# Performance work log

Measured on AMD Instinct MI355X. Metric: run time of the kernel, lower is better.

## Reference

```python
import jax, jax.numpy as jnp
import numpy as np


def _sobel_filters():
    # 3D Sobel kernels for x, y, z directions, shape (3, 1, 3, 3, 3) in OIDHW.
    x = np.array([[[-1, 0, 1], [-2, 0, 2], [-1, 0, 1]],
                  [[-2, 0, 2], [-4, 0, 4], [-2, 0, 2]],
                  [[-1, 0, 1], [-2, 0, 2], [-1, 0, 1]]], dtype=np.float32)
    y = np.array([[[1, 2, 1], [0, 0, 0], [-1, -2, -1]],
                  [[2, 4, 2], [0, 0, 0], [-2, -4, -2]],
                  [[1, 2, 1], [0, 0, 0], [-1, -2, -1]]], dtype=np.float32)
    z = np.array([[[1, 2, 1], [2, 4, 2], [1, 2, 1]],
                  [[0, 0, 0], [0, 0, 0], [0, 0, 0]],
                  [[-1, -2, -1], [-2, -4, -2], [-1, -2, -1]]], dtype=np.float32)
    return jnp.asarray(np.stack([x, y, z])[:, None])  # (3,1,3,3,3)


_FILTERS = _sobel_filters()
_EPS = 1e-10


def gradient3d(x):
    # x: [B,1,D,H,W] -> gradient magnitude [B,1,D,H,W].
    # Single conv with 3 output channels == three separate torch conv3d + concat.
    g = jax.lax.conv_general_dilated(
        x, _FILTERS, window_strides=(1, 1, 1),
        padding=[(1, 1), (1, 1), (1, 1)],
        dimension_numbers=('NCDHW', 'OIDHW', 'NCDHW'))  # [B,3,D,H,W]
    return jnp.sqrt(jnp.sum(g * g, axis=1, keepdims=True) + _EPS)


def setup_inputs() -> dict:
    key = jax.random.key(0)
    k1, k2, k3 = jax.random.split(key, 3)
    shape = (2, 1, 192, 192, 192)
    pred = jax.random.normal(k1, shape, dtype=jnp.float32)
    gt_dose = jax.random.normal(k2, shape, dtype=jnp.float32)
    body_mask = (jax.random.uniform(k3, shape) > 0.3).astype(jnp.float32)
    return {"pred": pred, "gt_dose": gt_dose, "body_mask": body_mask}


def reference(pred, gt_dose, body_mask):
    mse = jnp.square(pred - gt_dose) * body_mask
    mge = jnp.square(gradient3d(gt_dose) - gradient3d(pred)) * body_mask
    return jnp.mean(mse + jnp.tanh(mge) * mse)
```

## Files before the change

kernel.cpp:

```cpp
#include <hip/hip_runtime.h>
#include <math.h>

#define W 192
#define H 192
#define DEPTH 192
#define BATCH 2
#define TW 64
#define TH 8
#define DC 12
#define HW (H * W)
#define VOL ((size_t)DEPTH * HW)
#define LROW 72
#define LPLANE (LROW * 10)
#define NPAIR ((DC + 2) / 2)
#define NITEM 720

__global__ __launch_bounds__(256) void sobel_loss_part(
    const float* __restrict__ pred, const float* __restrict__ gt,
    const float* __restrict__ mask, float* __restrict__ partials)
{
    __shared__ __align__(16) float lds[2 * 2 * LPLANE];

    const int tid = threadIdx.x;
    const int tx = blockIdx.x % 3;
    const int ty = blockIdx.x / 3;
    const int w0 = tx * TW, h0 = ty * TH;
    const int d0 = blockIdx.y * DC;
    const size_t base = (size_t)blockIdx.z * VOL;

    const int wv  = tid >> 6;
    const int col = tid & 63;
    const size_t moff = base + (size_t)(h0 + 2 * wv) * W + (w0 + col);

    int it_ok[3], it_st[3], it_q[3], it_lds[3];
    size_t it_goff[3];
    const float* it_src[3];
    #pragma unroll
    for (int k = 0; k < 3; ++k) {
        int j = tid + 256 * k;
        int jj = (j < NITEM) ? j : 0;
        int a = jj / 360; int pj = jj - a * 360;
        int q = pj / 180; int e = pj - q * 180;
        int r = e / 18;   int c = e - r * 18;
        int y  = h0 - 1 + r;
        int xf = w0 - 4 + 4 * c;
        it_st[k]  = (j < NITEM);
        it_ok[k]  = it_st[k] && ((unsigned)y < (unsigned)H) && ((unsigned)xf < (unsigned)W);
        it_goff[k] = it_ok[k] ? ((size_t)y * W + xf) : 0;
        it_lds[k]  = ((a * 2 + q) * 10 + r) * LROW + 4 * c;
        it_q[k]    = q;
        it_src[k]  = a ? gt : pred;
    }

    float4 R[3];
    auto load_pair = [&](int s) {
        const int p0 = d0 - 1 + 2 * s;
        #pragma unroll
        for (int k = 0; k < 3; ++k) {
            const int p = p0 + it_q[k];
            const bool v = it_ok[k] && (p >= 0) && (p < DEPTH);
            R[k] = v ? *(const float4*)(it_src[k] + base + (size_t)p * HW + it_goff[k])
                     : make_float4(0.f, 0.f, 0.f, 0.f);
        }
    };

    float2 Mn = make_float2(0.f, 0.f), Mn1 = make_float2(0.f, 0.f);
    float2 Mc, Mc1;
    auto load_mask = [&](int s) {
        const size_t p0 = moff + (size_t)(d0 + 2 * s - 2) * HW;
        Mn  = make_float2(mask[p0], mask[p0 + W]);
        Mn1 = make_float2(mask[p0 + HW], mask[p0 + HW + W]);
    };

    float dx[2][2][3], dy[2][2][3], sm[2][2][3], ct[2][2][2];
    #pragma unroll
    for (int a = 0; a < 2; ++a)
        #pragma unroll
        for (int o = 0; o < 2; ++o) {
            dx[a][o][0]=dx[a][o][1]=dx[a][o][2]=0.f;
            dy[a][o][0]=dy[a][o][1]=dy[a][o][2]=0.f;
            sm[a][o][0]=sm[a][o][1]=sm[a][o][2]=0.f;
            ct[a][o][0]=ct[a][o][1]=0.f;
        }
    float acc = 0.f;

    load_pair(0);

    for (int s = 0; s < NPAIR; ++s) {
        __syncthreads();
        #pragma unroll
        for (int k = 0; k < 3; ++k)
            if (it_st[k]) *(float4*)(lds + it_lds[k]) = R[k];
        __syncthreads();

        Mc = Mn; Mc1 = Mn1;
        if (s + 1 < NPAIR) {
            load_pair(s + 1);
            load_mask(s + 1);
        }

        #pragma unroll
        for (int q = 0; q < 2; ++q) {
            const int p = d0 - 1 + 2 * s + q;

            #pragma unroll
            for (int a = 0; a < 2; ++a) {
                const int ab = (a * 2 + q) * LPLANE + (2 * wv) * LROW + col + 3;
                float e[4][3];
                #pragma unroll
                for (int rr = 0; rr < 4; ++rr)
                    #pragma unroll
                    for (int d = 0; d < 3; ++d)
                        e[rr][d] = lds[ab + rr * LROW + d];

                float rs[4], rd[4];
                #pragma unroll
                for (int rr = 0; rr < 4; ++rr) {
                    rs[rr] = e[rr][0] + 2.f * e[rr][1] + e[rr][2];
                    rd[rr] = e[rr][2] - e[rr][0];
                }
                #pragma unroll
                for (int o = 0; o < 2; ++o) {
                    dx[a][o][0] = dx[a][o][1]; dx[a][o][1] = dx[a][o][2];
                    dx[a][o][2] = rd[o] + 2.f * rd[o+1] + rd[o+2];
                    sm[a][o][0] = sm[a][o][1]; sm[a][o][1] = sm[a][o][2];
                    sm[a][o][2] = rs[o] + 2.f * rs[o+1] + rs[o+2];
                    dy[a][o][0] = dy[a][o][1]; dy[a][o][1] = dy[a][o][2];
                    dy[a][o][2] = rs[o] - rs[o+2];
                    ct[a][o][0] = ct[a][o][1]; ct[a][o][1] = e[o+1][1];
                }
            }

            if (p >= d0 + 1) {
                const float2 M = q ? Mc1 : Mc;
                #pragma unroll
                for (int o = 0; o < 2; ++o) {
                    float gxa = dx[0][o][0] + 2.f * dx[0][o][1] + dx[0][o][2];
                    float gya = dy[0][o][0] + 2.f * dy[0][o][1] + dy[0][o][2];
                    float gza = sm[0][o][0] - sm[0][o][2];
                    float gxb = dx[1][o][0] + 2.f * dx[1][o][1] + dx[1][o][2];
                    float gyb = dy[1][o][0] + 2.f * dy[1][o][1] + dy[1][o][2];
                    float gzb = sm[1][o][0] - sm[1][o][2];
                    float ga = __builtin_amdgcn_sqrtf(gxa * gxa + gya * gya + gza * gza + 1e-10f);
                    float gb = __builtin_amdgcn_sqrtf(gxb * gxb + gyb * gyb + gzb * gzb + 1e-10f);
                    float m  = o ? M.y : M.x;
                    float dm = ct[0][o][0] - ct[1][o][0];
                    float mse = dm * dm * m;
                    float dg  = gb - ga;
                    float mge = dg * dg * m;
                    float ex = __expf(2.f * mge);
                    float t  = 1.f - 2.f * __builtin_amdgcn_rcpf(ex + 1.f);
                    acc += mse * (1.f + t);
                }
            }
        }
    }

    float v = acc;
    #pragma unroll
    for (int o = 32; o > 0; o >>= 1) v += __shfl_down(v, o, 64);
    __shared__ float red[4];
    if ((tid & 63) == 0) red[tid >> 6] = v;
    __syncthreads();
    if (tid == 0) {
        partials[(size_t)blockIdx.z * (gridDim.x * gridDim.y)
                 + (size_t)blockIdx.y * gridDim.x + blockIdx.x]
            = red[0] + red[1] + red[2] + red[3];
    }
}

__global__ __launch_bounds__(256) void reduce_final(
    const float* __restrict__ partials, int n, float* __restrict__ out)
{
    int tid = threadIdx.x;
    double s = 0.0;
    for (int i = tid; i < n; i += 256) s += (double)partials[i];
    #pragma unroll
    for (int o = 32; o > 0; o >>= 1) s += __shfl_down(s, o, 64);
    __shared__ double red[4];
    if ((tid & 63) == 0) red[tid >> 6] = s;
    __syncthreads();
    if (tid == 0) {
        double t = red[0] + red[1] + red[2] + red[3];
        const double ntot = (double)BATCH * (double)DEPTH * (double)H * (double)W;
        out[0] = (float)(t / ntot);
    }
}

extern "C" void kernel_launch(void* const* d_in, const int* in_sizes, int n_in,
                              void* d_out, int out_size, void* d_ws, size_t ws_size,
                              hipStream_t stream) {
    const float* pred = (const float*)d_in[0];
    const float* gt   = (const float*)d_in[1];
    const float* mask = (const float*)d_in[2];
    float* partials = (float*)d_ws;

    dim3 grid((W / TW) * (H / TH), DEPTH / DC, BATCH);
    sobel_loss_part<<<grid, 256, 0, stream>>>(pred, gt, mask, partials);

    int nparts = grid.x * grid.y * grid.z;
    reduce_final<<<1, 256, 0, stream>>>(partials, nparts, (float*)d_out);
}
```

Baseline: 185.0 us.

## Stream input planes into LDS with async global_load_lds triple buffering

Result: no change. 186.8 us (+1.0%).

```diff
diff --git a/kernel.cpp b/kernel.cpp
--- a/kernel.cpp
+++ b/kernel.cpp
@@ -14,12 +14,17 @@
 #define LPLANE (LROW * 10)
 #define NPAIR ((DC + 2) / 2)
 #define NITEM 720
+#define NBUF 3
+#define BUFFLOATS 3072
+
+__device__ __align__(16) float g_zero16[16] = {0.f};
 
 __global__ __launch_bounds__(256) void sobel_loss_part(
     const float* __restrict__ pred, const float* __restrict__ gt,
     const float* __restrict__ mask, float* __restrict__ partials)
 {
-    __shared__ __align__(16) float lds[2 * 2 * LPLANE];
+    __shared__ __align__(16) float lds[NBUF * BUFFLOATS];
+    __shared__ float red[4];
 
     const int tid = threadIdx.x;
     const int tx = blockIdx.x % 3;
@@ -32,7 +37,7 @@
     const int col = tid & 63;
     const size_t moff = base + (size_t)(h0 + 2 * wv) * W + (w0 + col);
 
-    int it_ok[3], it_st[3], it_q[3], it_lds[3];
+    int it_ok[3], it_q[3];
     size_t it_goff[3];
     const float* it_src[3];
     #pragma unroll
@@ -44,23 +49,26 @@
         int r = e / 18;   int c = e - r * 18;
         int y  = h0 - 1 + r;
         int xf = w0 - 4 + 4 * c;
-        it_st[k]  = (j < NITEM);
-        it_ok[k]  = it_st[k] && ((unsigned)y < (unsigned)H) && ((unsigned)xf < (unsigned)W);
+        it_ok[k]  = (j < NITEM) && ((unsigned)y < (unsigned)H) && ((unsigned)xf < (unsigned)W);
         it_goff[k] = it_ok[k] ? ((size_t)y * W + xf) : 0;
-        it_lds[k]  = ((a * 2 + q) * 10 + r) * LROW + 4 * c;
         it_q[k]    = q;
         it_src[k]  = a ? gt : pred;
     }
 
-    float4 R[3];
-    auto load_pair = [&](int s) {
+    typedef const __attribute__((address_space(1))) void GV;
+    typedef __attribute__((address_space(3))) void LV;
+
+    auto dma_pair = [&](int s) {
+        float* bufp = lds + (s % NBUF) * BUFFLOATS;
         const int p0 = d0 - 1 + 2 * s;
         #pragma unroll
         for (int k = 0; k < 3; ++k) {
             const int p = p0 + it_q[k];
             const bool v = it_ok[k] && (p >= 0) && (p < DEPTH);
-            R[k] = v ? *(const float4*)(it_src[k] + base + (size_t)p * HW + it_goff[k])
-                     : make_float4(0.f, 0.f, 0.f, 0.f);
+            const float* ga = v ? (it_src[k] + base + (size_t)p * HW + it_goff[k])
+                               : g_zero16;
+            __builtin_amdgcn_global_load_lds((GV*)ga,
+                (LV*)(bufp + (((wv << 6) + (k << 8)) << 2)), 16, 0, 0);
         }
     };
 
@@ -84,20 +92,25 @@
         }
     float acc = 0.f;
 
-    load_pair(0);
+    dma_pair(0);
+    dma_pair(1);
 
     for (int s = 0; s < NPAIR; ++s) {
-        __syncthreads();
-        #pragma unroll
-        for (int k = 0; k < 3; ++k)
-            if (it_st[k]) *(float4*)(lds + it_lds[k]) = R[k];
-        __syncthreads();
+        if (s < NPAIR - 1) {
+            asm volatile("s_waitcnt vmcnt(3)" ::: "memory");
+        } else {
+            asm volatile("s_waitcnt vmcnt(0)" ::: "memory");
+        }
+        __builtin_amdgcn_sched_barrier(0);
+        __builtin_amdgcn_s_barrier();
+        __builtin_amdgcn_sched_barrier(0);
+
+        if (s + 2 < NPAIR) dma_pair(s + 2);
 
         Mc = Mn; Mc1 = Mn1;
-        if (s + 1 < NPAIR) {
-            load_pair(s + 1);
-            load_mask(s + 1);
-        }
+        if (s + 1 < NPAIR) load_mask(s + 1);
+
+        const float* buf = lds + (s % NBUF) * BUFFLOATS;
 
         #pragma unroll
         for (int q = 0; q < 2; ++q) {
@@ -111,7 +124,7 @@
                 for (int rr = 0; rr < 4; ++rr)
                     #pragma unroll
                     for (int d = 0; d < 3; ++d)
-                        e[rr][d] = lds[ab + rr * LROW + d];
+                        e[rr][d] = buf[ab + rr * LROW + d];
 
                 float rs[4], rd[4];
                 #pragma unroll
@@ -159,7 +172,6 @@
     float v = acc;
     #pragma unroll
     for (int o = 32; o > 0; o >>= 1) v += __shfl_down(v, o, 64);
-    __shared__ float red[4];
     if ((tid & 63) == 0) red[tid >> 6] = v;
     __syncthreads();
     if (tid == 0) {
```

## Replace LDS-staged tile loads with direct clamped global loads per thread

Applied to the files above, without the earlier changes.

Measured after the change: 189.4 us. +2.4%, slower.

```diff
diff --git a/kernel.cpp b/kernel.cpp
--- a/kernel.cpp
+++ b/kernel.cpp
@@ -10,17 +10,15 @@
 #define DC 12
 #define HW (H * W)
 #define VOL ((size_t)DEPTH * HW)
-#define LROW 72
-#define LPLANE (LROW * 10)
-#define NPAIR ((DC + 2) / 2)
-#define NITEM 720
+#define NPL (DC + 2)
+#define GX ((W / TW) * (H / TH))
+#define GY (DEPTH / DC)
+#define NBLK (GX * GY * BATCH)
 
 __global__ __launch_bounds__(256) void sobel_loss_part(
     const float* __restrict__ pred, const float* __restrict__ gt,
     const float* __restrict__ mask, float* __restrict__ partials)
 {
-    __shared__ __align__(16) float lds[2 * 2 * LPLANE];
-
     const int tid = threadIdx.x;
     const int tx = blockIdx.x % 3;
     const int ty = blockIdx.x / 3;
@@ -30,47 +28,25 @@
 
     const int wv  = tid >> 6;
     const int col = tid & 63;
-    const size_t moff = base + (size_t)(h0 + 2 * wv) * W + (w0 + col);
+    const int colg = w0 + col;
+    const int ra = h0 + 2 * wv;
 
-    int it_ok[3], it_st[3], it_q[3], it_lds[3];
-    size_t it_goff[3];
-    const float* it_src[3];
+    int yoff[4]; float rmask[4];
     #pragma unroll
-    for (int k = 0; k < 3; ++k) {
-        int j = tid + 256 * k;
-        int jj = (j < NITEM) ? j : 0;
-        int a = jj / 360; int pj = jj - a * 360;
-        int q = pj / 180; int e = pj - q * 180;
-        int r = e / 18;   int c = e - r * 18;
-        int y  = h0 - 1 + r;
-        int xf = w0 - 4 + 4 * c;
-        it_st[k]  = (j < NITEM);
-        it_ok[k]  = it_st[k] && ((unsigned)y < (unsigned)H) && ((unsigned)xf < (unsigned)W);
-        it_goff[k] = it_ok[k] ? ((size_t)y * W + xf) : 0;
-        it_lds[k]  = ((a * 2 + q) * 10 + r) * LROW + 4 * c;
-        it_q[k]    = q;
-        it_src[k]  = a ? gt : pred;
+    for (int r = 0; r < 4; ++r) {
+        int y = ra - 1 + r;
+        rmask[r] = ((unsigned)y < (unsigned)H) ? 1.f : 0.f;
+        int yc = y < 0 ? 0 : (y > H - 1 ? H - 1 : y);
+        yoff[r] = yc * W;
     }
+    const float lmk = (colg > 0)     ? 1.f : 0.f;
+    const float rmk = (colg < W - 1) ? 1.f : 0.f;
+    const int cl = colg > 0     ? colg - 1 : 0;
+    const int cr = colg < W - 1 ? colg + 1 : W - 1;
 
-    float4 R[3];
-    auto load_pair = [&](int s) {
-        const int p0 = d0 - 1 + 2 * s;
-        #pragma unroll
-        for (int k = 0; k < 3; ++k) {
-            const int p = p0 + it_q[k];
-            const bool v = it_ok[k] && (p >= 0) && (p < DEPTH);
-            R[k] = v ? *(const float4*)(it_src[k] + base + (size_t)p * HW + it_goff[k])
-                     : make_float4(0.f, 0.f, 0.f, 0.f);
-        }
-    };
-
-    float2 Mn = make_float2(0.f, 0.f), Mn1 = make_float2(0.f, 0.f);
-    float2 Mc, Mc1;
-    auto load_mask = [&](int s) {
-        const size_t p0 = moff + (size_t)(d0 + 2 * s - 2) * HW;
-        Mn  = make_float2(mask[p0], mask[p0 + W]);
-        Mn1 = make_float2(mask[p0 + HW], mask[p0 + HW + W]);
-    };
+    const float* __restrict__ A0 = pred + base;
+    const float* __restrict__ A1 = gt + base;
+    const float* __restrict__ MB = mask + base + (size_t)ra * W + colg;
 
     float dx[2][2][3], dy[2][2][3], sm[2][2][3], ct[2][2][2];
     #pragma unroll
@@ -83,77 +59,77 @@
             ct[a][o][0]=ct[a][o][1]=0.f;
         }
     float acc = 0.f;
+    float2 Mc = make_float2(0.f, 0.f), Mn = make_float2(0.f, 0.f);
 
-    load_pair(0);
+    #pragma unroll
+    for (int i = 0; i < NPL; ++i) {
+        const int p = d0 - 1 + i;
+        const float pm = ((unsigned)p < (unsigned)DEPTH) ? 1.f : 0.f;
+        const int  pc = p < 0 ? 0 : (p > DEPTH - 1 ? DEPTH - 1 : p);
+        const size_t pb = (size_t)pc * HW;
 
-    for (int s = 0; s < NPAIR; ++s) {
-        __syncthreads();
+        if (i >= 1 && i <= DC) {
+            const float* mp = MB + (size_t)p * HW;
+            Mn = make_float2(mp[0], mp[W]);
+        }
+
+        float msk[4];
         #pragma unroll
-        for (int k = 0; k < 3; ++k)
-            if (it_st[k]) *(float4*)(lds + it_lds[k]) = R[k];
-        __syncthreads();
+        for (int r = 0; r < 4; ++r) msk[r] = rmask[r] * pm;
 
-        Mc = Mn; Mc1 = Mn1;
-        if (s + 1 < NPAIR) {
-            load_pair(s + 1);
-            load_mask(s + 1);
+        float rs[2][4], rd[2][4], cc[2][2];
+        #pragma unroll
+        for (int a = 0; a < 2; ++a) {
+            const float* src = (a ? A1 : A0) + pb;
+            #pragma unroll
+            for (int r = 0; r < 4; ++r) {
+                const float* rp = src + yoff[r];
+                float m = rp[colg];
+                float l = rp[cl] * lmk;
+                float q = rp[cr] * rmk;
+                rs[a][r] = msk[r] * (l + 2.f * m + q);
+                rd[a][r] = msk[r] * (q - l);
+                if (r == 1) cc[a][0] = msk[r] * m;
+                if (r == 2) cc[a][1] = msk[r] * m;
+            }
         }
 
         #pragma unroll
-        for (int q = 0; q < 2; ++q) {
-            const int p = d0 - 1 + 2 * s + q;
-
+        for (int a = 0; a < 2; ++a)
             #pragma unroll
-            for (int a = 0; a < 2; ++a) {
-                const int ab = (a * 2 + q) * LPLANE + (2 * wv) * LROW + col + 3;
-                float e[4][3];
-                #pragma unroll
-                for (int rr = 0; rr < 4; ++rr)
-                    #pragma unroll
-                    for (int d = 0; d < 3; ++d)
-                        e[rr][d] = lds[ab + rr * LROW + d];
-
-                float rs[4], rd[4];
-                #pragma unroll
-                for (int rr = 0; rr < 4; ++rr) {
-                    rs[rr] = e[rr][0] + 2.f * e[rr][1] + e[rr][2];
-                    rd[rr] = e[rr][2] - e[rr][0];
-                }
-                #pragma unroll
-                for (int o = 0; o < 2; ++o) {
-                    dx[a][o][0] = dx[a][o][1]; dx[a][o][1] = dx[a][o][2];
-                    dx[a][o][2] = rd[o] + 2.f * rd[o+1] + rd[o+2];
-                    sm[a][o][0] = sm[a][o][1]; sm[a][o][1] = sm[a][o][2];
-                    sm[a][o][2] = rs[o] + 2.f * rs[o+1] + rs[o+2];
-                    dy[a][o][0] = dy[a][o][1]; dy[a][o][1] = dy[a][o][2];
-                    dy[a][o][2] = rs[o] - rs[o+2];
-                    ct[a][o][0] = ct[a][o][1]; ct[a][o][1] = e[o+1][1];
-                }
+            for (int o = 0; o < 2; ++o) {
+                dx[a][o][0] = dx[a][o][1]; dx[a][o][1] = dx[a][o][2];
+                dx[a][o][2] = rd[a][o] + 2.f * rd[a][o+1] + rd[a][o+2];
+                sm[a][o][0] = sm[a][o][1]; sm[a][o][1] = sm[a][o][2];
+                sm[a][o][2] = rs[a][o] + 2.f * rs[a][o+1] + rs[a][o+2];
+                dy[a][o][0] = dy[a][o][1]; dy[a][o][1] = dy[a][o][2];
+                dy[a][o][2] = rs[a][o] - rs[a][o+2];
+                ct[a][o][0] = ct[a][o][1]; ct[a][o][1] = cc[a][o];
             }
 
-            if (p >= d0 + 1) {
-                const float2 M = q ? Mc1 : Mc;
-                #pragma unroll
-                for (int o = 0; o < 2; ++o) {
-                    float gxa = dx[0][o][0] + 2.f * dx[0][o][1] + dx[0][o][2];
-                    float gya = dy[0][o][0] + 2.f * dy[0][o][1] + dy[0][o][2];
-                    float gza = sm[0][o][0] - sm[0][o][2];
-                    float gxb = dx[1][o][0] + 2.f * dx[1][o][1] + dx[1][o][2];
-                    float gyb = dy[1][o][0] + 2.f * dy[1][o][1] + dy[1][o][2];
-                    float gzb = sm[1][o][0] - sm[1][o][2];
-                    float ga = __builtin_amdgcn_sqrtf(gxa * gxa + gya * gya + gza * gza + 1e-10f);
-                    float gb = __builtin_amdgcn_sqrtf(gxb * gxb + gyb * gyb + gzb * gzb + 1e-10f);
-                    float m  = o ? M.y : M.x;
-                    float dm = ct[0][o][0] - ct[1][o][0];
-                    float mse = dm * dm * m;
-                    float dg  = gb - ga;
-                    float mge = dg * dg * m;
-                    float ex = __expf(2.f * mge);
-                    float t  = 1.f - 2.f * __builtin_amdgcn_rcpf(ex + 1.f);
-                    acc += mse * (1.f + t);
-                }
+        if (i >= 2) {
+            const float2 M = Mc;
+            #pragma unroll
+            for (int o = 0; o < 2; ++o) {
+                float gxa = dx[0][o][0] + 2.f * dx[0][o][1] + dx[0][o][2];
+                float gya = dy[0][o][0] + 2.f * dy[0][o][1] + dy[0][o][2];
+                float gza = sm[0][o][0] - sm[0][o][2];
+                float gxb = dx[1][o][0] + 2.f * dx[1][o][1] + dx[1][o][2];
+                float gyb = dy[1][o][0] + 2.f * dy[1][o][1] + dy[1][o][2];
+                float gzb = sm[1][o][0] - sm[1][o][2];
+                float ga = __builtin_amdgcn_sqrtf(gxa * gxa + gya * gya + gza * gza + 1e-10f);
+                float gb = __builtin_amdgcn_sqrtf(gxb * gxb + gyb * gyb + gzb * gzb + 1e-10f);
+                float m  = o ? M.y : M.x;
+                float dm = ct[0][o][0] - ct[1][o][0];
+                float mse = dm * dm * m;
+                float dg  = gb - ga;
+                float mge = dg * dg * m;
+                float ex = __expf(2.f * mge);
+                float t  = 1.f - 2.f * __builtin_amdgcn_rcpf(ex + 1.f);
+                acc += mse * (1.f + t);
             }
         }
+        Mc = Mn;
     }
 
     float v = acc;
@@ -163,8 +139,8 @@
     if ((tid & 63) == 0) red[tid >> 6] = v;
     __syncthreads();
     if (tid == 0) {
-        partials[(size_t)blockIdx.z * (gridDim.x * gridDim.y)
-                 + (size_t)blockIdx.y * gridDim.x + blockIdx.x]
+        partials[(size_t)blockIdx.z * (GX * GY)
+                 + (size_t)blockIdx.y * GX + blockIdx.x]
             = red[0] + red[1] + red[2] + red[3];
     }
 }
@@ -195,9 +171,8 @@
     const float* mask = (const float*)d_in[2];
     float* partials = (float*)d_ws;
 
-    dim3 grid((W / TW) * (H / TH), DEPTH / DC, BATCH);
+    dim3 grid(GX, GY, BATCH);
     sobel_loss_part<<<grid, 256, 0, stream>>>(pred, gt, mask, partials);
 
-    int nparts = grid.x * grid.y * grid.z;
-    reduce_final<<<1, 256, 0, stream>>>(partials, nparts, (float*)d_out);
+    reduce_final<<<1, 256, 0, stream>>>(partials, NBLK, (float*)d_out);
 }
```
